# Optimization experiments

Measured on AMD Instinct MI355X. Metric: run time of the kernel, lower is better.

Reference implementation:

```python
import jax, jax.numpy as jnp
import numpy as np

B, C, H, W = 4, 96, 64, 64
D_STATE, D_CONV, EXPAND = 16, 4, 2
D_INNER = EXPAND * C          # 192
DT_RANK = (C + 15) // 16      # 6
BN_EPS = 1e-5


def setup_inputs() -> dict:
    key = jax.random.key(0)
    ks = jax.random.split(key, 10)
    s = 0.02
    return {
        "x": jax.random.normal(ks[0], (B, C, H, W), jnp.float32),
        # Mamba block params (mamba_ssm layout, no bias on in/out proj)
        "in_proj_w": jax.random.normal(ks[1], (2 * D_INNER, C), jnp.float32) * s,
        "conv1d_w": jax.random.normal(ks[2], (D_INNER, 1, D_CONV), jnp.float32) * s,  # depthwise
        "conv1d_b": jnp.zeros((D_INNER,), jnp.float32),
        "x_proj_w": jax.random.normal(ks[3], (DT_RANK + 2 * D_STATE, D_INNER), jnp.float32) * s,
        "dt_proj_w": jax.random.normal(ks[4], (D_INNER, DT_RANK), jnp.float32) * s,
        "dt_proj_b": jax.random.normal(ks[5], (D_INNER,), jnp.float32) * s,
        "A_log": jnp.log(jnp.tile(jnp.arange(1, D_STATE + 1, dtype=jnp.float32), (D_INNER, 1))),
        "D": jnp.ones((D_INNER,), jnp.float32),
        "out_proj_w": jax.random.normal(ks[6], (C, D_INNER), jnp.float32) * s,
        # trailing ConvBNReLU6 params
        "conv2d_w": jax.random.normal(ks[7], (C, C, 3, 3), jnp.float32) * s,
        "bn_gamma": jnp.ones((C,), jnp.float32),
        "bn_beta": jnp.zeros((C,), jnp.float32),
        "bn_mean": jnp.zeros((C,), jnp.float32),
        "bn_var": jnp.ones((C,), jnp.float32),
    }


def _forward(x, in_proj_w, conv1d_w, conv1d_b, x_proj_w, dt_proj_w, dt_proj_b,
             A_log, D, out_proj_w, conv2d_w, bn_gamma, bn_beta, bn_mean, bn_var):
    b, c, h, w = x.shape
    L = h * w
    seq = x.reshape(b, c, L).transpose(0, 2, 1)              # [B, L, C] tokens
    xz = seq @ in_proj_w.T                                    # [B, L, 2*D_INNER]
    xi, z = jnp.split(xz, 2, axis=-1)

    # depthwise causal conv1d + SiLU
    xi_c = jax.lax.conv_general_dilated(
        xi.transpose(0, 2, 1), conv1d_w, (1,), [(D_CONV - 1, 0)],
        dimension_numbers=("NCH", "OIH", "NCH"), feature_group_count=D_INNER)
    xi = jax.nn.silu((xi_c + conv1d_b[None, :, None]).transpose(0, 2, 1))  # [B, L, D_INNER]

    # input-dependent dt, B, C
    x_dbl = xi @ x_proj_w.T                                   # [B, L, DT_RANK + 2*D_STATE]
    dt, Bm, Cm = jnp.split(x_dbl, [DT_RANK, DT_RANK + D_STATE], axis=-1)
    dt = jax.nn.softplus(dt @ dt_proj_w.T + dt_proj_b)        # [B, L, D_INNER]

    # discretize: dA = exp(dt*A), dBx = dt*B*x
    A = -jnp.exp(A_log)                                       # [D_INNER, D_STATE]
    dA = jnp.exp(dt[..., None] * A)                           # [B, L, D_INNER, D_STATE]
    dBx = dt[..., None] * Bm[:, :, None, :] * xi[..., None]   # [B, L, D_INNER, D_STATE]

    def step(hst, inputs):
        dA_t, dBx_t, C_t = inputs
        hst = dA_t * hst + dBx_t                              # [B, D_INNER, D_STATE]
        y_t = jnp.einsum("bds,bs->bd", hst, C_t)
        return hst, y_t

    h0 = jnp.zeros((b, D_INNER, D_STATE), xi.dtype)
    _, ys = jax.lax.scan(step, h0,
                         (dA.transpose(1, 0, 2, 3), dBx.transpose(1, 0, 2, 3), Cm.transpose(1, 0, 2)))
    y = ys.transpose(1, 0, 2)                                 # [B, L, D_INNER]
    y = (y + xi * D) * jax.nn.silu(z)                         # skip D + gate
    out = y @ out_proj_w.T                                    # [B, L, C]
    xm = out.transpose(0, 2, 1).reshape(b, c, h, w)

    # ConvBNReLU: 3x3 conv (pad 1, no bias) -> BN (inference) -> ReLU6
    xo = jax.lax.conv_general_dilated(xm, conv2d_w, (1, 1), [(1, 1), (1, 1)],
                                      dimension_numbers=("NCHW", "OIHW", "NCHW"))
    inv = bn_gamma / jnp.sqrt(bn_var + BN_EPS)
    xo = xo * inv[None, :, None, None] + (bn_beta - bn_mean * inv)[None, :, None, None]
    return jnp.clip(xo, 0.0, 6.0)


def reference(x, in_proj_w, conv1d_w, conv1d_b, x_proj_w, dt_proj_w, dt_proj_b,
              A_log, D, out_proj_w, conv2d_w, bn_gamma, bn_beta, bn_mean, bn_var):
    return _forward(x, in_proj_w, conv1d_w, conv1d_b, x_proj_w, dt_proj_w, dt_proj_b,
                    A_log, D, out_proj_w, conv2d_w, bn_gamma, bn_beta, bn_mean, bn_var)
```

## Files before the change

### kernel.cpp

```cpp
#include <hip/hip_runtime.h>
#include <math.h>

#define LQ 4096
#define DI 192
#define DS 16
#define NCHUNK 64

__device__ __forceinline__ float siluf_(float v) { return v / (1.f + __expf(-v)); }
__device__ __forceinline__ float softplusf_(float v) { return v > 20.f ? v : log1pf(__expf(v)); }

template <int CTRL>
__device__ __forceinline__ float dpp_add16_(float x) {
    int y = __builtin_amdgcn_update_dpp(0, __float_as_int(x), CTRL, 0xf, 0xf, true);
    return x + __int_as_float(y);
}
template <int CTRL>
__device__ __forceinline__ float dpp_shift_(float x) {
    int y = __builtin_amdgcn_update_dpp(0, __float_as_int(x), CTRL, 0xf, 0xf, true);
    return __int_as_float(y);
}
__device__ __forceinline__ void async_g2l16_(const float* g, float* l) {
    __builtin_amdgcn_global_load_lds(
        (const __attribute__((address_space(1))) void*)g,
        (__attribute__((address_space(3))) void*)l, 16, 0, 0);
}
__device__ __forceinline__ void async_g2l4_(const float* g, float* l) {
    __builtin_amdgcn_global_load_lds(
        (const __attribute__((address_space(1))) void*)g,
        (__attribute__((address_space(3))) void*)l, 4, 0, 0);
}

__global__ __launch_bounds__(256) void k1_inproj(const float* __restrict__ x,
    const float* __restrict__ w, float* __restrict__ xi_raw, float* __restrict__ z)
{
    const int l0 = blockIdx.x * 64;
    const int n0 = blockIdx.y * 64;
    const int b  = blockIdx.z;
    __shared__ float xs[96 * 64];
    __shared__ float wsT[96 * 68];
    const int tid = threadIdx.x;
    for (int i = tid; i < 96 * 16; i += 256) {
        int c = i >> 4, lq = i & 15;
        *(float4*)&xs[c * 64 + lq * 4] =
            *(const float4*)&x[(b * 96 + c) * LQ + l0 + lq * 4];
    }
    for (int i = tid; i < 64 * 24; i += 256) {
        int n = i / 24, cq = i - n * 24;
        float4 v = *(const float4*)&w[(n0 + n) * 96 + cq * 4];
        wsT[(cq * 4 + 0) * 68 + n] = v.x;
        wsT[(cq * 4 + 1) * 68 + n] = v.y;
        wsT[(cq * 4 + 2) * 68 + n] = v.z;
        wsT[(cq * 4 + 3) * 68 + n] = v.w;
    }
    __syncthreads();
    const int tx = tid & 15;
    const int ty = tid >> 4;
    float acc[4][4];
#pragma unroll
    for (int i = 0; i < 4; ++i)
#pragma unroll
        for (int j = 0; j < 4; ++j) acc[i][j] = 0.f;
    for (int k = 0; k < 96; ++k) {
        float4 a  = *(const float4*)&xs[k * 64 + ty * 4];
        float4 bb = *(const float4*)&wsT[k * 68 + tx * 4];
        float av[4] = {a.x, a.y, a.z, a.w};
        float bv[4] = {bb.x, bb.y, bb.z, bb.w};
#pragma unroll
        for (int i = 0; i < 4; ++i)
#pragma unroll
            for (int j = 0; j < 4; ++j) acc[i][j] += av[i] * bv[j];
    }
    float* dst = (n0 < DI) ? xi_raw : z;
    const int nn0 = (n0 < DI) ? n0 : (n0 - DI);
#pragma unroll
    for (int i = 0; i < 4; ++i) {
        int l = l0 + ty * 4 + i;
        float4 v = make_float4(acc[i][0], acc[i][1], acc[i][2], acc[i][3]);
        *(float4*)&dst[(b * LQ + l) * DI + nn0 + tx * 4] = v;
    }
}

__global__ __launch_bounds__(256) void k2_conv1d(const float* __restrict__ xir,
    const float* __restrict__ cw, const float* __restrict__ cb, float* __restrict__ xi)
{
    int idx = blockIdx.x * 256 + threadIdx.x;
    int d = idx % DI;
    int l = (idx / DI) & (LQ - 1);
    float4 wv = *(const float4*)&cw[d * 4];
    float wk[4] = {wv.x, wv.y, wv.z, wv.w};
    float acc = cb[d];
#pragma unroll
    for (int k = 0; k < 4; ++k) {
        int lp = l - 3 + k;
        if (lp >= 0) acc += wk[k] * xir[idx + (k - 3) * DI];
    }
    xi[idx] = siluf_(acc);
}

__global__ __launch_bounds__(256) void k3_xdbl(const float* __restrict__ xi,
    const float* __restrict__ xw, float* __restrict__ xdbl)
{
    const int l0 = blockIdx.x * 64;
    const int b  = blockIdx.y;
    __shared__ float sxiT[96 * 68];
    __shared__ float swx[38 * 196];
    const int tid = threadIdx.x;
    for (int i = tid; i < 38 * 48; i += 256) {
        int n = i / 48, kq = i - n * 48;
        *(float4*)&swx[n * 196 + kq * 4] = *(const float4*)&xw[n * 192 + kq * 4];
    }
    const int lq = tid & 15, ng = tid >> 4;
    float acc[3][4];
#pragma unroll
    for (int p = 0; p < 3; ++p)
#pragma unroll
        for (int i = 0; i < 4; ++i) acc[p][i] = 0.f;
    for (int half = 0; half < 2; ++half) {
        __syncthreads();
        for (int i = tid; i < 64 * 24; i += 256) {
            int l = i / 24, kq = i - l * 24;
            float4 v = *(const float4*)&xi[(b * LQ + l0 + l) * DI + half * 96 + kq * 4];
            sxiT[(kq * 4 + 0) * 68 + l] = v.x;
            sxiT[(kq * 4 + 1) * 68 + l] = v.y;
            sxiT[(kq * 4 + 2) * 68 + l] = v.z;
            sxiT[(kq * 4 + 3) * 68 + l] = v.w;
        }
        __syncthreads();
#pragma unroll
        for (int pass = 0; pass < 3; ++pass) {
            int n = pass * 16 + ng;
            if (n >= 38) continue;
            for (int k = 0; k < 96; ++k) {
                float4 a = *(const float4*)&sxiT[k * 68 + lq * 4];
                float bv = swx[n * 196 + half * 96 + k];
                acc[pass][0] += a.x * bv;
                acc[pass][1] += a.y * bv;
                acc[pass][2] += a.z * bv;
                acc[pass][3] += a.w * bv;
            }
        }
    }
#pragma unroll
    for (int pass = 0; pass < 3; ++pass) {
        int n = pass * 16 + ng;
        if (n >= 38) continue;
#pragma unroll
        for (int i = 0; i < 4; ++i)
            xdbl[(b * LQ + l0 + lq * 4 + i) * 38 + n] = acc[pass][i];
    }
}

__global__ __launch_bounds__(256) void k4_scanA(
    const float* __restrict__ xdbl, const float* __restrict__ xi,
    const float* __restrict__ dtw, const float* __restrict__ dtb,
    const float* __restrict__ alog,
    float* __restrict__ cA, float* __restrict__ cB)
{
    const int ch = blockIdx.x, g = blockIdx.y, b = blockIdx.z;
    const int t0 = ch * 64, d0 = g * 16;
    __shared__ float sxd[64 * 40];
    __shared__ float sdt[1024], sxi[1024];
    __shared__ float sdtw[96], sdtb[16];
    const int tid = threadIdx.x;
    for (int i = tid; i < 64 * 38; i += 256) {
        int t = i / 38, cc = i - t * 38;
        sxd[t * 40 + cc] = xdbl[(b * LQ + t0 + t) * 38 + cc];
    }
    for (int i = tid; i < 1024; i += 256) {
        int t = i >> 4, j = i & 15;
        sxi[i] = xi[(b * LQ + t0 + t) * DI + d0 + j];
    }
    if (tid < 96) sdtw[tid] = dtw[d0 * 6 + tid];
    if (tid < 16) sdtb[tid] = dtb[d0 + tid];
    __syncthreads();
    for (int i = tid; i < 1024; i += 256) {
        int t = i >> 4, dl = i & 15;
        float acc = sdtb[dl];
#pragma unroll
        for (int r = 0; r < 6; ++r) acc += sxd[t * 40 + r] * sdtw[dl * 6 + r];
        sdt[i] = softplusf_(acc);
    }
    __syncthreads();
    const int s = tid & 15, dl = tid >> 4;
    const float Ads = -__expf(alog[(d0 + dl) * DS + s]);
    float a = 1.f, hb = 0.f;
#pragma unroll 4
    for (int t = 0; t < 64; ++t) {
        float dtv = sdt[t * 16 + dl];
        float dA = __expf(dtv * Ads);
        float dbx = dtv * sxd[t * 40 + 6 + s] * sxi[t * 16 + dl];
        a *= dA;
        hb = dA * hb + dbx;
    }
    int o = ((b * NCHUNK + ch) * DI + d0 + dl) * DS + s;
    cA[o] = a;
    cB[o] = hb;
}

__global__ __launch_bounds__(256) void k5_combine(const float* __restrict__ cA,
    const float* __restrict__ cB, float* __restrict__ hinit)
{
    int gid = blockIdx.x * 256 + threadIdx.x;
    int b = gid / 3072;
    int rem = gid - b * 3072;
    int base = b * (NCHUNK * 3072) + rem;
    float h = 0.f;
#pragma unroll 8
    for (int c = 0; c < NCHUNK; ++c) {
        int o = base + c * 3072;
        hinit[o] = h;
        h = cA[o] * h + cB[o];
    }
}

__global__ __launch_bounds__(256) void k6_scanC(
    const float* __restrict__ xdbl, const float* __restrict__ xi,
    const float* __restrict__ z, const float* __restrict__ dtw,
    const float* __restrict__ dtb, const float* __restrict__ alog,
    const float* __restrict__ Dp, const float* __restrict__ hinit,
    float* __restrict__ yg)
{
    const int ch = blockIdx.x, g = blockIdx.y, b = blockIdx.z;
    const int t0 = ch * 64, d0 = g * 16;
    __shared__ float sxd[64 * 40];
    __shared__ float sdt[1024], sxi[1024], szs[1024], sy[1024];
    __shared__ float sdtw[96], sdtb[16];
    const int tid = threadIdx.x;
    for (int i = tid; i < 64 * 38; i += 256) {
        int t = i / 38, cc = i - t * 38;
        sxd[t * 40 + cc] = xdbl[(b * LQ + t0 + t) * 38 + cc];
    }
    for (int i = tid; i < 1024; i += 256) {
        int t = i >> 4, j = i & 15;
        int row = b * LQ + t0 + t;
        sxi[i] = xi[row * DI + d0 + j];
        szs[i] = z[row * DI + d0 + j];
    }
    if (tid < 96) sdtw[tid] = dtw[d0 * 6 + tid];
    if (tid < 16) sdtb[tid] = dtb[d0 + tid];
    __syncthreads();
    for (int i = tid; i < 1024; i += 256) {
        int t = i >> 4, dl = i & 15;
        float acc = sdtb[dl];
#pragma unroll
        for (int r = 0; r < 6; ++r) acc += sxd[t * 40 + r] * sdtw[dl * 6 + r];
        sdt[i] = softplusf_(acc);
    }
    __syncthreads();
    const int s = tid & 15, dl = tid >> 4;
    const float Ads = -__expf(alog[(d0 + dl) * DS + s]);
    float h = hinit[((b * NCHUNK + ch) * DI + d0 + dl) * DS + s];
    for (int t = 0; t < 64; ++t) {
        float dtv = sdt[t * 16 + dl];
        float dA = __expf(dtv * Ads);
        h = dA * h + dtv * sxd[t * 40 + 6 + s] * sxi[t * 16 + dl];
        float p = h * sxd[t * 40 + 22 + s];
        p = dpp_add16_<0x128>(p);
        p = dpp_add16_<0x124>(p);
        p = dpp_add16_<0x122>(p);
        p = dpp_add16_<0x121>(p);
        if (s == 0) sy[t * 16 + dl] = p;
    }
    __syncthreads();
    for (int i = tid; i < 1024; i += 256) {
        int t = i >> 4, j = i & 15;
        float gate = siluf_(szs[i]);
        yg[(b * LQ + t0 + t) * DI + d0 + j] = (sy[i] + sxi[i] * Dp[d0 + j]) * gate;
    }
}

__global__ __launch_bounds__(256) void k7_outproj(const float* __restrict__ yg,
    const float* __restrict__ wo, float* __restrict__ xm)
{
    const int l0 = blockIdx.x * 64;
    const int n0 = blockIdx.y * 32;
    const int b  = blockIdx.z;
    __shared__ float syT[96 * 68];
    __shared__ float wtT[192 * 36];
    const int tid = threadIdx.x;
    for (int i = tid; i < 32 * 48; i += 256) {
        int n = i / 48, kq = i - n * 48;
        float4 v = *(const float4*)&wo[(n0 + n) * DI + kq * 4];
        wtT[(kq * 4 + 0) * 36 + n] = v.x;
        wtT[(kq * 4 + 1) * 36 + n] = v.y;
        wtT[(kq * 4 + 2) * 36 + n] = v.z;
        wtT[(kq * 4 + 3) * 36 + n] = v.w;
    }
    const int tx = tid & 15;
    const int ty = tid >> 4;
    float acc[2][4];
#pragma unroll
    for (int j = 0; j < 2; ++j)
#pragma unroll
        for (int i = 0; i < 4; ++i) acc[j][i] = 0.f;
    for (int half = 0; half < 2; ++half) {
        __syncthreads();
        for (int i = tid; i < 64 * 24; i += 256) {
            int l = i / 24, kq = i - l * 24;
            float4 v = *(const float4*)&yg[(b * LQ + l0 + l) * DI + half * 96 + kq * 4];
            syT[(kq * 4 + 0) * 68 + l] = v.x;
            syT[(kq * 4 + 1) * 68 + l] = v.y;
            syT[(kq * 4 + 2) * 68 + l] = v.z;
            syT[(kq * 4 + 3) * 68 + l] = v.w;
        }
        __syncthreads();
        for (int k = 0; k < 96; ++k) {
            float4 a = *(const float4*)&syT[k * 68 + tx * 4];
            int kk = half * 96 + k;
            float b0 = wtT[kk * 36 + ty * 2 + 0];
            float b1 = wtT[kk * 36 + ty * 2 + 1];
            acc[0][0] += a.x * b0; acc[0][1] += a.y * b0;
            acc[0][2] += a.z * b0; acc[0][3] += a.w * b0;
            acc[1][0] += a.x * b1; acc[1][1] += a.y * b1;
            acc[1][2] += a.z * b1; acc[1][3] += a.w * b1;
        }
    }
#pragma unroll
    for (int j = 0; j < 2; ++j) {
        float4 v = make_float4(acc[j][0], acc[j][1], acc[j][2], acc[j][3]);
        *(float4*)&xm[(b * 96 + n0 + ty * 2 + j) * LQ + l0 + tx * 4] = v;
    }
}

#define K8_INQ 384
#define K8_WNEL 576
__global__ __launch_bounds__(256) void k8_conv3(const float* __restrict__ xm,
    const float* __restrict__ w2, float* __restrict__ pbuf)
{
    const int ks  = blockIdx.x & 3;
    const int co0 = (blockIdx.x >> 2) * 16;
    const int y0  = blockIdx.y * 4;
    const int b   = blockIdx.z;
    __shared__ float sin2[2][1536];
    __shared__ float swt2[2][576];
    const int tid = threadIdx.x;
    const int sx = tid & 15;
    const int sy = (tid >> 4) & 3;
    const int cq = tid >> 6;

    int in_goff[2];
    bool in_ok[2];
#pragma unroll
    for (int j = 0; j < 2; ++j) {
        int i = tid + j * 256;
        int ci  = i / 96;
        int rem = i - ci * 96;
        int row = rem >> 4;
        int qx  = rem & 15;
        int gy  = y0 + row - 1;
        bool ok = (i < K8_INQ) && gy >= 0 && gy < 64;
        in_ok[j]  = ok;
        in_goff[j] = ok ? (ci * 4096 + gy * 64 + qx * 4) : 0;
    }
    int w_goff[3];
#pragma unroll
    for (int j = 0; j < 3; ++j) {
        int i = tid + j * 256;
        int ci  = i / 144;
        int rem = i - ci * 144;
        int k   = rem >> 4;
        int cl  = rem & 15;
        w_goff[j] = (i < K8_WNEL) ? (cl * 864 + ci * 9 + k) : 0;
    }

    const float* xb = xm + (size_t)b * 96 * 4096 + (size_t)ks * 24 * 4096;
    const float* wb = w2 + (size_t)co0 * 864 + ks * 24 * 9;
    const float4 zero4 = make_float4(0.f, 0.f, 0.f, 0.f);

#pragma unroll
    for (int bu = 0; bu < 2; ++bu) {
        if (!in_ok[0]) *(float4*)&sin2[bu][tid * 4] = zero4;
        if (tid < 128 && !in_ok[1]) *(float4*)&sin2[bu][(256 + tid) * 4] = zero4;
    }

    {
        const float* gx = xb;
        const float* gw = wb;
        if (in_ok[0]) async_g2l16_(gx + in_goff[0], &sin2[0][cq * 256]);
        if (tid < 128 && in_ok[1]) async_g2l16_(gx + in_goff[1], &sin2[0][1024 + cq * 256]);
        async_g2l4_(gw + w_goff[0], &swt2[0][cq * 64]);
        async_g2l4_(gw + w_goff[1], &swt2[0][256 + cq * 64]);
        if (tid < 64) async_g2l4_(gw + w_goff[2], &swt2[0][512 + cq * 64]);
    }
    __syncthreads();

    float acc[4][4];
#pragma unroll
    for (int c = 0; c < 4; ++c)
#pragma unroll
        for (int x = 0; x < 4; ++x) acc[c][x] = 0.f;

#pragma clang loop unroll(disable)
    for (int ch = 0; ch < 6; ++ch) {
        if (ch < 5) {
            const int nb = (ch + 1) & 1;
            const float* gx = xb + (ch + 1) * 16384;
            const float* gw = wb + (ch + 1) * 36;
            if (in_ok[0]) async_g2l16_(gx + in_goff[0], &sin2[nb][cq * 256]);
            if (tid < 128 && in_ok[1]) async_g2l16_(gx + in_goff[1], &sin2[nb][1024 + cq * 256]);
            async_g2l4_(gw + w_goff[0], &swt2[nb][cq * 64]);
            async_g2l4_(gw + w_goff[1], &swt2[nb][256 + cq * 64]);
            if (tid < 64) async_g2l4_(gw + w_goff[2], &swt2[nb][512 + cq * 64]);
        }

        const float* sc = sin2[ch & 1];
        const float* wc = swt2[ch & 1];
#pragma unroll
        for (int cii = 0; cii < 4; ++cii) {
            float w6[3][6];
#pragma unroll
            for (int r = 0; r < 3; ++r) {
                float4 v = *(const float4*)&sc[(cii * 6 + sy + r) * 64 + sx * 4];
                w6[r][0] = dpp_shift_<0x111>(v.w);
                w6[r][1] = v.x; w6[r][2] = v.y; w6[r][3] = v.z; w6[r][4] = v.w;
                w6[r][5] = dpp_shift_<0x101>(v.x);
            }
#pragma unroll
            for (int ky = 0; ky < 3; ++ky) {
#pragma unroll
                for (int kx = 0; kx < 3; ++kx) {
                    float4 wv = *(const float4*)&wc[(cii * 9 + ky * 3 + kx) * 16 + cq * 4];
#pragma unroll
                    for (int x = 0; x < 4; ++x) {
                        float pv = w6[ky][x + kx];
                        acc[0][x] = fmaf(pv, wv.x, acc[0][x]);
                        acc[1][x] = fmaf(pv, wv.y, acc[1][x]);
                        acc[2][x] = fmaf(pv, wv.z, acc[2][x]);
                        acc[3][x] = fmaf(pv, wv.w, acc[3][x]);
                    }
                }
            }
        }

        __syncthreads();
    }

    const int yy = y0 + sy;
    float* pb = pbuf + (size_t)ks * 1572864;
#pragma unroll
    for (int c = 0; c < 4; ++c) {
        const int cc = co0 + cq * 4 + c;
        float4 o = make_float4(acc[c][0], acc[c][1], acc[c][2], acc[c][3]);
        *(float4*)&pb[((size_t)(b * 96 + cc) * 64 + yy) * 64 + sx * 4] = o;
    }
}

__global__ __launch_bounds__(256) void k9_reduce(const float* __restrict__ pbuf,
    const float* __restrict__ bng, const float* __restrict__ bnb,
    const float* __restrict__ bnm, const float* __restrict__ bnv,
    float* __restrict__ out)
{
    const int q = blockIdx.x * 256 + threadIdx.x;
    const int idx = q * 4;
    const int c = (idx >> 12) % 96;
    float4 s = *(const float4*)&pbuf[idx];
    float4 s1 = *(const float4*)&pbuf[idx + 1572864];
    float4 s2 = *(const float4*)&pbuf[idx + 2 * 1572864];
    float4 s3 = *(const float4*)&pbuf[idx + 3 * 1572864];
    s.x += s1.x + s2.x + s3.x;
    s.y += s1.y + s2.y + s3.y;
    s.z += s1.z + s2.z + s3.z;
    s.w += s1.w + s2.w + s3.w;
    float inv = bng[c] / sqrtf(bnv[c] + 1e-5f);
    float add = bnb[c] - bnm[c] * inv;
    float4 o;
    o.x = fminf(fmaxf(s.x * inv + add, 0.f), 6.f);
    o.y = fminf(fmaxf(s.y * inv + add, 0.f), 6.f);
    o.z = fminf(fmaxf(s.z * inv + add, 0.f), 6.f);
    o.w = fminf(fmaxf(s.w * inv + add, 0.f), 6.f);
    *(float4*)&out[idx] = o;
}

extern "C" void kernel_launch(void* const* d_in, const int* in_sizes, int n_in,
                              void* d_out, int out_size, void* d_ws, size_t ws_size,
                              hipStream_t stream) {
    (void)in_sizes; (void)n_in; (void)out_size; (void)ws_size;
    const float* x    = (const float*)d_in[0];
    const float* w_in = (const float*)d_in[1];
    const float* cw   = (const float*)d_in[2];
    const float* cb   = (const float*)d_in[3];
    const float* xw   = (const float*)d_in[4];
    const float* dtw  = (const float*)d_in[5];
    const float* dtb  = (const float*)d_in[6];
    const float* alog = (const float*)d_in[7];
    const float* Dp   = (const float*)d_in[8];
    const float* wo   = (const float*)d_in[9];
    const float* w2   = (const float*)d_in[10];
    const float* bng  = (const float*)d_in[11];
    const float* bnb  = (const float*)d_in[12];
    const float* bnm  = (const float*)d_in[13];
    const float* bnv  = (const float*)d_in[14];

    float* ws = (float*)d_ws;
    float* xi_raw = ws;
    float* z      = ws + 3145728;
    float* xi     = ws + 6291456;
    float* xdbl   = ws + 9437184;
    float* cA     = ws + 10059776;
    float* cB     = ws + 10846208;
    float* hinit  = ws + 11632640;
    float* xm     = ws + 12419072;
    float* yg     = xi_raw;
    float* pbuf   = xi_raw;

    dim3 blk(256);
    k1_inproj<<<dim3(64, 6, 4), blk, 0, stream>>>(x, w_in, xi_raw, z);
    k2_conv1d<<<dim3(12288), blk, 0, stream>>>(xi_raw, cw, cb, xi);
    k3_xdbl<<<dim3(64, 4), blk, 0, stream>>>(xi, xw, xdbl);
    k4_scanA<<<dim3(NCHUNK, 12, 4), blk, 0, stream>>>(xdbl, xi, dtw, dtb, alog, cA, cB);
    k5_combine<<<dim3(48), blk, 0, stream>>>(cA, cB, hinit);
    k6_scanC<<<dim3(NCHUNK, 12, 4), blk, 0, stream>>>(xdbl, xi, z, dtw, dtb, alog, Dp, hinit, yg);
    k7_outproj<<<dim3(64, 3, 4), blk, 0, stream>>>(yg, wo, xm);
    k8_conv3<<<dim3(24, 16, 4), blk, 0, stream>>>(xm, w2, pbuf);
    k9_reduce<<<dim3(1536), blk, 0, stream>>>(pbuf, bng, bnb, bnm, bnv, (float*)d_out);
}
```

Measured before the change: 281.5 us.

## Restructure chunked scan: one thread per channel holding all 16 states in registers

```diff
diff --git a/kernel.cpp b/kernel.cpp
--- a/kernel.cpp
+++ b/kernel.cpp
@@ -4,16 +4,12 @@
 #define LQ 4096
 #define DI 192
 #define DS 16
-#define NCHUNK 64
+#define NCH 128
+#define TCH 32
 
 __device__ __forceinline__ float siluf_(float v) { return v / (1.f + __expf(-v)); }
 __device__ __forceinline__ float softplusf_(float v) { return v > 20.f ? v : log1pf(__expf(v)); }
 
-template <int CTRL>
-__device__ __forceinline__ float dpp_add16_(float x) {
-    int y = __builtin_amdgcn_update_dpp(0, __float_as_int(x), CTRL, 0xf, 0xf, true);
-    return x + __int_as_float(y);
-}
 template <int CTRL>
 __device__ __forceinline__ float dpp_shift_(float x) {
     int y = __builtin_amdgcn_update_dpp(0, __float_as_int(x), CTRL, 0xf, 0xf, true);
@@ -150,122 +146,139 @@
     }
 }
 
-__global__ __launch_bounds__(256) void k4_scanA(
+__global__ __launch_bounds__(192) void k4_scanA(
     const float* __restrict__ xdbl, const float* __restrict__ xi,
     const float* __restrict__ dtw, const float* __restrict__ dtb,
     const float* __restrict__ alog,
     float* __restrict__ cA, float* __restrict__ cB)
 {
-    const int ch = blockIdx.x, g = blockIdx.y, b = blockIdx.z;
-    const int t0 = ch * 64, d0 = g * 16;
-    __shared__ float sxd[64 * 40];
-    __shared__ float sdt[1024], sxi[1024];
-    __shared__ float sdtw[96], sdtb[16];
-    const int tid = threadIdx.x;
-    for (int i = tid; i < 64 * 38; i += 256) {
+    const int ch = blockIdx.x, b = blockIdx.y;
+    const int t0 = ch * TCH;
+    __shared__ float sxd[TCH * 40];
+    const int d = threadIdx.x;
+    for (int i = d; i < TCH * 38; i += 192) {
         int t = i / 38, cc = i - t * 38;
         sxd[t * 40 + cc] = xdbl[(b * LQ + t0 + t) * 38 + cc];
     }
-    for (int i = tid; i < 1024; i += 256) {
-        int t = i >> 4, j = i & 15;
-        sxi[i] = xi[(b * LQ + t0 + t) * DI + d0 + j];
-    }
-    if (tid < 96) sdtw[tid] = dtw[d0 * 6 + tid];
-    if (tid < 16) sdtb[tid] = dtb[d0 + tid];
+    float dtw6[6];
+#pragma unroll
+    for (int r = 0; r < 6; ++r) dtw6[r] = dtw[d * 6 + r];
+    const float dtbd = dtb[d];
+    float Ads[16];
+#pragma unroll
+    for (int s = 0; s < 16; ++s) Ads[s] = -__expf(alog[d * 16 + s]);
+    float a[16], hb[16];
+#pragma unroll
+    for (int s = 0; s < 16; ++s) { a[s] = 1.f; hb[s] = 0.f; }
     __syncthreads();
-    for (int i = tid; i < 1024; i += 256) {
-        int t = i >> 4, dl = i & 15;
-        float acc = sdtb[dl];
-#pragma unroll
-        for (int r = 0; r < 6; ++r) acc += sxd[t * 40 + r] * sdtw[dl * 6 + r];
-        sdt[i] = softplusf_(acc);
-    }
-    __syncthreads();
-    const int s = tid & 15, dl = tid >> 4;
-    const float Ads = -__expf(alog[(d0 + dl) * DS + s]);
-    float a = 1.f, hb = 0.f;
-#pragma unroll 4
-    for (int t = 0; t < 64; ++t) {
-        float dtv = sdt[t * 16 + dl];
-        float dA = __expf(dtv * Ads);
-        float dbx = dtv * sxd[t * 40 + 6 + s] * sxi[t * 16 + dl];
-        a *= dA;
-        hb = dA * hb + dbx;
-    }
-    int o = ((b * NCHUNK + ch) * DI + d0 + dl) * DS + s;
-    cA[o] = a;
-    cB[o] = hb;
-}
-
-__global__ __launch_bounds__(256) void k5_combine(const float* __restrict__ cA,
-    const float* __restrict__ cB, float* __restrict__ hinit)
+    float xiv_next = xi[(b * LQ + t0) * DI + d];
+    for (int t = 0; t < TCH; ++t) {
+        float xiv = xiv_next;
+        if (t + 1 < TCH) xiv_next = xi[(b * LQ + t0 + t + 1) * DI + d];
+        float acc = dtbd;
+#pragma unroll
+        for (int r = 0; r < 6; ++r) acc = fmaf(sxd[t * 40 + r], dtw6[r], acc);
+        float dtv = softplusf_(acc);
+        float dtxi = dtv * xiv;
+        const float* Bp = &sxd[t * 40 + 6];
+#pragma unroll
+        for (int s = 0; s < 16; ++s) {
+            float dA = __expf(dtv * Ads[s]);
+            a[s] *= dA;
+            hb[s] = fmaf(dA, hb[s], dtxi * Bp[s]);
+        }
+    }
+    int o = ((b * NCH + ch) * DI + d) * 16;
+#pragma unroll
+    for (int s = 0; s < 16; s += 4) {
+        *(float4*)&cA[o + s] = make_float4(a[s], a[s + 1], a[s + 2], a[s + 3]);
+        *(float4*)&cB[o + s] = make_float4(hb[s], hb[s + 1], hb[s + 2], hb[s + 3]);
+    }
+}
+
+__global__ __launch_bounds__(256) void k5_combine(const float* cA,
+    const float* __restrict__ cB, float* hinit)
 {
     int gid = blockIdx.x * 256 + threadIdx.x;
     int b = gid / 3072;
     int rem = gid - b * 3072;
-    int base = b * (NCHUNK * 3072) + rem;
+    int base = b * (NCH * 3072) + rem;
     float h = 0.f;
 #pragma unroll 8
-    for (int c = 0; c < NCHUNK; ++c) {
+    for (int c = 0; c < NCH; ++c) {
         int o = base + c * 3072;
+        float av = cA[o];
+        float bv = cB[o];
         hinit[o] = h;
-        h = cA[o] * h + cB[o];
-    }
-}
-
-__global__ __launch_bounds__(256) void k6_scanC(
+        h = fmaf(av, h, bv);
+    }
+}
+
+__global__ __launch_bounds__(192) void k6_scanC(
     const float* __restrict__ xdbl, const float* __restrict__ xi,
     const float* __restrict__ z, const float* __restrict__ dtw,
     const float* __restrict__ dtb, const float* __restrict__ alog,
     const float* __restrict__ Dp, const float* __restrict__ hinit,
     float* __restrict__ yg)
 {
-    const int ch = blockIdx.x, g = blockIdx.y, b = blockIdx.z;
-    const int t0 = ch * 64, d0 = g * 16;
-    __shared__ float sxd[64 * 40];
-    __shared__ float sdt[1024], sxi[1024], szs[1024], sy[1024];
-    __shared__ float sdtw[96], sdtb[16];
-    const int tid = threadIdx.x;
-    for (int i = tid; i < 64 * 38; i += 256) {
+    const int ch = blockIdx.x, b = blockIdx.y;
+    const int t0 = ch * TCH;
+    __shared__ float sxd[TCH * 40];
+    const int d = threadIdx.x;
+    for (int i = d; i < TCH * 38; i += 192) {
         int t = i / 38, cc = i - t * 38;
         sxd[t * 40 + cc] = xdbl[(b * LQ + t0 + t) * 38 + cc];
     }
-    for (int i = tid; i < 1024; i += 256) {
-        int t = i >> 4, j = i & 15;
-        int row = b * LQ + t0 + t;
-        sxi[i] = xi[row * DI + d0 + j];
-        szs[i] = z[row * DI + d0 + j];
-    }
-    if (tid < 96) sdtw[tid] = dtw[d0 * 6 + tid];
-    if (tid < 16) sdtb[tid] = dtb[d0 + tid];
+    float dtw6[6];
+#pragma unroll
+    for (int r = 0; r < 6; ++r) dtw6[r] = dtw[d * 6 + r];
+    const float dtbd = dtb[d];
+    const float Dd = Dp[d];
+    float Ads[16];
+#pragma unroll
+    for (int s = 0; s < 16; ++s) Ads[s] = -__expf(alog[d * 16 + s]);
+    float h[16];
+    const int o = ((b * NCH + ch) * DI + d) * 16;
+#pragma unroll
+    for (int s = 0; s < 16; s += 4) {
+        float4 v = *(const float4*)&hinit[o + s];
+        h[s] = v.x; h[s + 1] = v.y; h[s + 2] = v.z; h[s + 3] = v.w;
+    }
     __syncthreads();
-    for (int i = tid; i < 1024; i += 256) {
-        int t = i >> 4, dl = i & 15;
-        float acc = sdtb[dl];
-#pragma unroll
-        for (int r = 0; r < 6; ++r) acc += sxd[t * 40 + r] * sdtw[dl * 6 + r];
-        sdt[i] = softplusf_(acc);
-    }
-    __syncthreads();
-    const int s = tid & 15, dl = tid >> 4;
-    const float Ads = -__expf(alog[(d0 + dl) * DS + s]);
-    float h = hinit[((b * NCHUNK + ch) * DI + d0 + dl) * DS + s];
-    for (int t = 0; t < 64; ++t) {
-        float dtv = sdt[t * 16 + dl];
-        float dA = __expf(dtv * Ads);
-        h = dA * h + dtv * sxd[t * 40 + 6 + s] * sxi[t * 16 + dl];
-        float p = h * sxd[t * 40 + 22 + s];
-        p = dpp_add16_<0x128>(p);
-        p = dpp_add16_<0x124>(p);
-        p = dpp_add16_<0x122>(p);
-        p = dpp_add16_<0x121>(p);
-        if (s == 0) sy[t * 16 + dl] = p;
-    }
-    __syncthreads();
-    for (int i = tid; i < 1024; i += 256) {
-        int t = i >> 4, j = i & 15;
-        float gate = siluf_(szs[i]);
-        yg[(b * LQ + t0 + t) * DI + d0 + j] = (sy[i] + sxi[i] * Dp[d0 + j]) * gate;
+    float xiv_next = xi[(b * LQ + t0) * DI + d];
+    float zv_next  = z[(b * LQ + t0) * DI + d];
+    for (int t = 0; t < TCH; ++t) {
+        float xiv = xiv_next, zv = zv_next;
+        if (t + 1 < TCH) {
+            xiv_next = xi[(b * LQ + t0 + t + 1) * DI + d];
+            zv_next  = z[(b * LQ + t0 + t + 1) * DI + d];
+        }
+        float acc = dtbd;
+#pragma unroll
+        for (int r = 0; r < 6; ++r) acc = fmaf(sxd[t * 40 + r], dtw6[r], acc);
+        float dtv = softplusf_(acc);
+        float dtxi = dtv * xiv;
+        const float* Bp = &sxd[t * 40 + 6];
+        const float* Cp = &sxd[t * 40 + 22];
+        float y0 = 0.f, y1 = 0.f, y2 = 0.f, y3 = 0.f;
+#pragma unroll
+        for (int s = 0; s < 16; s += 4) {
+            float dA0 = __expf(dtv * Ads[s]);
+            float dA1 = __expf(dtv * Ads[s + 1]);
+            float dA2 = __expf(dtv * Ads[s + 2]);
+            float dA3 = __expf(dtv * Ads[s + 3]);
+            h[s]     = fmaf(dA0, h[s],     dtxi * Bp[s]);
+            h[s + 1] = fmaf(dA1, h[s + 1], dtxi * Bp[s + 1]);
+            h[s + 2] = fmaf(dA2, h[s + 2], dtxi * Bp[s + 2]);
+            h[s + 3] = fmaf(dA3, h[s + 3], dtxi * Bp[s + 3]);
+            y0 = fmaf(h[s],     Cp[s],     y0);
+            y1 = fmaf(h[s + 1], Cp[s + 1], y1);
+            y2 = fmaf(h[s + 2], Cp[s + 2], y2);
+            y3 = fmaf(h[s + 3], Cp[s + 3], y3);
+        }
+        float y = (y0 + y1) + (y2 + y3);
+        float gate = siluf_(zv);
+        yg[(b * LQ + t0 + t) * DI + d] = (y + xiv * Dd) * gate;
     }
 }
 
@@ -431,7 +444,6 @@
                 }
             }
         }
-
         __syncthreads();
     }
 
@@ -497,9 +509,9 @@
     float* xi     = ws + 6291456;
     float* xdbl   = ws + 9437184;
     float* cA     = ws + 10059776;
-    float* cB     = ws + 10846208;
-    float* hinit  = ws + 11632640;
-    float* xm     = ws + 12419072;
+    float* cB     = ws + 11632640;
+    float* hinit  = cA;
+    float* xm     = cB;
     float* yg     = xi_raw;
     float* pbuf   = xi_raw;
 
@@ -507,9 +519,9 @@
     k1_inproj<<<dim3(64, 6, 4), blk, 0, stream>>>(x, w_in, xi_raw, z);
     k2_conv1d<<<dim3(12288), blk, 0, stream>>>(xi_raw, cw, cb, xi);
     k3_xdbl<<<dim3(64, 4), blk, 0, stream>>>(xi, xw, xdbl);
-    k4_scanA<<<dim3(NCHUNK, 12, 4), blk, 0, stream>>>(xdbl, xi, dtw, dtb, alog, cA, cB);
+    k4_scanA<<<dim3(NCH, 4), dim3(192), 0, stream>>>(xdbl, xi, dtw, dtb, alog, cA, cB);
     k5_combine<<<dim3(48), blk, 0, stream>>>(cA, cB, hinit);
-    k6_scanC<<<dim3(NCHUNK, 12, 4), blk, 0, stream>>>(xdbl, xi, z, dtw, dtb, alog, Dp, hinit, yg);
+    k6_scanC<<<dim3(NCH, 4), dim3(192), 0, stream>>>(xdbl, xi, z, dtw, dtb, alog, Dp, hinit, yg);
     k7_outproj<<<dim3(64, 3, 4), blk, 0, stream>>>(yg, wo, xm);
     k8_conv3<<<dim3(24, 16, 4), blk, 0, stream>>>(xm, w2, pbuf);
     k9_reduce<<<dim3(1536), blk, 0, stream>>>(pbuf, bng, bnb, bnm, bnv, (float*)d_out);
```

Result: slower. 292.6 us (+4.0%).
